# Performance work log

Hardware: AMD Instinct MI355X
Metric: run time of the kernel (lower is better)

## Reference

```python
import jax, jax.numpy as jnp
import numpy as np
import math

B, N, D = 2, 192, 256

def _linear_params(key, d_in, d_out):
    kw, kb = jax.random.split(key)
    scale = 1.0 / math.sqrt(d_in)
    W = jax.random.uniform(kw, (d_out, d_in), jnp.float32, -scale, scale)
    b = jax.random.uniform(kb, (d_out,), jnp.float32, -scale, scale)
    return W, b

def setup_inputs() -> dict:
    key = jax.random.key(0)
    ks = jax.random.split(key, 7)
    Edges = jax.random.normal(ks[0], (B, N * N, D), jnp.float32)
    Wq_w, Wq_b = _linear_params(ks[1], D, D)
    Wk_w, Wk_b = _linear_params(ks[2], D, D)
    Wv_w, Wv_b = _linear_params(ks[3], D, D)
    Wb_w, Wb_b = _linear_params(ks[4], D, 1)
    Wg_w, Wg_b = _linear_params(ks[5], D, D)
    Wo_w, Wo_b = _linear_params(ks[6], D, D)
    return {"Edges": Edges, "Wq_w": Wq_w, "Wq_b": Wq_b, "Wk_w": Wk_w, "Wk_b": Wk_b,
            "Wv_w": Wv_w, "Wv_b": Wv_b, "Wb_w": Wb_w, "Wb_b": Wb_b,
            "Wg_w": Wg_w, "Wg_b": Wg_b, "Wo_w": Wo_w, "Wo_b": Wo_b}

def reference(Edges, Wq_w, Wq_b, Wk_w, Wk_b, Wv_w, Wv_b, Wb_w, Wb_b, Wg_w, Wg_b, Wo_w, Wo_b):
    # Edges: [B, N*N, D]; dropout is identity in eval mode.
    Bb, NN, Dd = Edges.shape
    n = int(round(math.sqrt(NN)))
    q = (Edges @ Wq_w.T + Wq_b).reshape(Bb, n, n, Dd)
    k = (Edges @ Wk_w.T + Wk_b).reshape(Bb, n, n, Dd)
    v = (Edges @ Wv_w.T + Wv_b).reshape(Bb, n, n, Dd)
    bmat = (Edges @ Wb_w.T + Wb_b).reshape(Bb, n, n)          # b[b,i,l]
    g = jax.nn.sigmoid(Edges @ Wg_w.T + Wg_b)                  # [B, N*N, D]
    # row attention: q(i,j) . k(i,l) ; column attention: q(i,j) . k(l,j)
    scores = (jnp.einsum('bijd,bild->bijl', q, k)
              + jnp.einsum('bijd,bljd->bijl', q, k)) / math.sqrt(Dd)
    sym_bias = bmat + jnp.swapaxes(bmat, 1, 2)                 # b[i,l] + b[l,i]
    alpha = jax.nn.softmax(scores + sym_bias[:, :, None, :], axis=-1)  # [B,n,n,n]
    # first value contraction along rows; second term matches torch's
    # transpose-free add: out2[b,i,j,d] = sum_l alpha[b,j,i,l] v[b,l,i,d]
    o1 = jnp.einsum('bijl,bild->bijd', alpha, v)
    o2 = jnp.einsum('bjil,blid->bijd', alpha, v)
    out = g * (o1 + o2).reshape(Bb, NN, Dd)
    out = jax.nn.relu(out @ Wo_w.T + Wo_b)
    return out
```

## Files before the change

kernel.cpp:

```cpp
#include <hip/hip_runtime.h>
#include <hip/hip_bf16.h>

typedef __hip_bfloat16 bf16;
typedef unsigned short u16;
typedef __attribute__((ext_vector_type(8))) short bf16x8;
typedef __attribute__((ext_vector_type(4))) float f32x4;

#define NB   2
#define NG   192
#define DD   256
#define NN2  (NG*NG)
#define MT   (NB*NN2)

static __device__ __forceinline__ float bfu2f(u16 u){
    return __uint_as_float(((unsigned)u) << 16);
}
static __device__ __forceinline__ u16 f2bfu(float f){
    bf16 h = __float2bfloat16(f);
    return *(u16*)&h;
}

static __device__ __forceinline__ void gl_lds16(const void* g, void* l){
    __builtin_amdgcn_global_load_lds(
        (const __attribute__((address_space(1))) unsigned int*)g,
        (__attribute__((address_space(3))) unsigned int*)l, 16, 0, 0);
}
static __device__ __forceinline__ int swz3(int x){ return ((x ^ (x>>3)) & 7) << 3; }

__global__ __launch_bounds__(256) void k_cast_eb(
    const float* __restrict__ E, const float* __restrict__ Wb,
    const float* __restrict__ bb, u16* __restrict__ Eb, float* __restrict__ bm)
{
    const int t = threadIdx.x;
    size_t base = (size_t)blockIdx.x*2048 + t*8;
    float4 x = *(const float4*)(E+base);
    float4 y = *(const float4*)(E+base+4);
    ushort4 a; a.x=f2bfu(x.x); a.y=f2bfu(x.y); a.z=f2bfu(x.z); a.w=f2bfu(x.w);
    ushort4 b; b.x=f2bfu(y.x); b.y=f2bfu(y.y); b.z=f2bfu(y.z); b.w=f2bfu(y.w);
    *(ushort4*)(Eb+base)   = a;
    *(ushort4*)(Eb+base+4) = b;
    const int l32 = t & 31;
    float4 w0 = ((const float4*)Wb)[l32*2];
    float4 w1 = ((const float4*)Wb)[l32*2+1];
    float s = x.x*w0.x + x.y*w0.y + x.z*w0.z + x.w*w0.w
            + y.x*w1.x + y.y*w1.y + y.z*w1.z + y.w*w1.w;
    #pragma unroll
    for (int off=1; off<32; off<<=1) s += __shfl_xor(s, off);
    if (l32 == 0) bm[blockIdx.x*8 + (t>>5)] = s + bb[0];
}

__global__ __launch_bounds__(256) void k_cast_w(
    const float* __restrict__ Wq, const float* __restrict__ Wk,
    const float* __restrict__ Wv, const float* __restrict__ Wg,
    const float* __restrict__ Wo,
    const float* __restrict__ bq, const float* __restrict__ bk,
    const float* __restrict__ bv, const float* __restrict__ bg,
    u16* __restrict__ Wcat, u16* __restrict__ Wob, float* __restrict__ biascat)
{
    int e = blockIdx.x*256 + threadIdx.x;
    Wcat[e]          = f2bfu(Wq[e]);
    Wcat[65536 + e]  = f2bfu(Wk[e]);
    Wcat[131072 + e] = f2bfu(Wv[e]);
    Wcat[196608 + e] = f2bfu(Wg[e]);
    Wob[e]           = f2bfu(Wo[e]);
    if (e < 1024){
        int p = e>>8, r = e&255;
        const float* bp = p==0?bq : p==1?bk : p==2?bv : bg;
        biascat[e] = bp[r];
    }
}

static __device__ __forceinline__ void gemm128_dbuf(
    const u16* __restrict__ A, const u16* __restrict__ B,
    u16* As, u16* Bs, f32x4 acc[4][4], int t)
{
    const int lane = t & 63, w = t >> 6;
    const int wm = (w>>1)*64, wn = (w&1)*64;
    int offA[4], offB[4];
    #pragma unroll
    for (int f=0; f<4; f++){
        int ra = wm + f*16 + (lane&15);
        offA[f] = ra*32 + (((lane>>4) ^ ((ra>>1)&3)) << 3);
        int rb = wn + f*16 + (lane&15);
        offB[f] = rb*32 + (((lane>>4) ^ ((rb>>1)&3)) << 3);
    }
    auto stage = [&](int buf, int k0){
        #pragma unroll
        for (int it=0; it<2; it++){
            int c = it*256 + t;
            int row = c >> 2;
            int ks  = (c&3) ^ ((row>>1)&3);
            gl_lds16(A + (size_t)row*DD + k0 + ks*8, As + buf*4096 + c*8);
            gl_lds16(B + (size_t)row*DD + k0 + ks*8, Bs + buf*4096 + c*8);
        }
    };
    stage(0, 0);
    for (int ks=0; ks<8; ks++){
        if (ks<7){
            stage((ks+1)&1, (ks+1)*32);
            asm volatile("s_waitcnt vmcnt(4)" ::: "memory");
        } else {
            asm volatile("s_waitcnt vmcnt(0)" ::: "memory");
        }
        __builtin_amdgcn_s_barrier();
        const u16* Ab = As + (ks&1)*4096;
        const u16* Bb = Bs + (ks&1)*4096;
        bf16x8 a[4], b[4];
        #pragma unroll
        for (int f=0; f<4; f++) a[f] = *(const bf16x8*)(Ab + offA[f]);
        #pragma unroll
        for (int f=0; f<4; f++) b[f] = *(const bf16x8*)(Bb + offB[f]);
        #pragma unroll
        for (int mf=0; mf<4; mf++)
            #pragma unroll
            for (int nf=0; nf<4; nf++)
                acc[mf][nf] = __builtin_amdgcn_mfma_f32_16x16x32_bf16(a[mf], b[nf], acc[mf][nf], 0, 0, 0);
        __builtin_amdgcn_s_barrier();
    }
}

__global__ __launch_bounds__(256) void k_proj_mfma(
    const u16* __restrict__ Eb, const u16* __restrict__ Wcat,
    const float* __restrict__ biascat,
    u16* __restrict__ qb, u16* __restrict__ kb,
    u16* __restrict__ vb, u16* __restrict__ gb)
{
    __shared__ u16 As[2*4096];
    __shared__ u16 Bs[2*4096];
    const int blk = blockIdx.x;
    const int xj = blk & 7, xi = blk >> 3;
    const int m0 = (xj*72 + (xi>>3)) * 128;
    const int n0 = (xi & 7) * 128;
    const int t = threadIdx.x, lane = t&63, w = t>>6;
    f32x4 acc[4][4];
    #pragma unroll
    for (int i=0;i<4;i++)
        #pragma unroll
        for (int j=0;j<4;j++) acc[i][j] = f32x4{0.f,0.f,0.f,0.f};
    gemm128_dbuf(Eb + (size_t)m0*DD, Wcat + (size_t)n0*DD, As, Bs, acc, t);

    const int p = n0 >> 8;
    u16* outp = p==0?qb : p==1?kb : p==2?vb : gb;
    const int wm = (w>>1)*64, wn = (w&1)*64;
    #pragma unroll
    for (int mf=0; mf<4; mf++){
        int m = m0 + wm + mf*16 + (lane>>4)*4;
        #pragma unroll
        for (int nf=0; nf<4; nf++){
            int gn = n0 + wn + nf*16 + (lane&15);
            float bias = biascat[gn];
            int col = gn & 255;
            #pragma unroll
            for (int r=0; r<4; r++){
                float v = acc[mf][nf][r] + bias;
                if (p==3) v = 1.0f/(1.0f+__expf(-v));
                outp[(size_t)(m+r)*DD + col] = f2bfu(v);
            }
        }
    }
}

__global__ __launch_bounds__(256) void k_final_mfma(
    const u16* __restrict__ hb, const u16* __restrict__ Wob,
    const float* __restrict__ bo, float* __restrict__ out)
{
    __shared__ u16 As[2*4096];
    __shared__ u16 Bs[2*4096];
    const int blk = blockIdx.x;
    const int xj = blk & 7, xi = blk >> 3;
    const int m0 = (xj*72 + (xi>>1)) * 128;
    const int n0 = (xi & 1) * 128;
    const int t = threadIdx.x, lane = t&63, w = t>>6;
    f32x4 acc[4][4];
    #pragma unroll
    for (int i=0;i<4;i++)
        #pragma unroll
        for (int j=0;j<4;j++) acc[i][j] = f32x4{0.f,0.f,0.f,0.f};
    gemm128_dbuf(hb + (size_t)m0*DD, Wob + (size_t)n0*DD, As, Bs, acc, t);

    const int wm = (w>>1)*64, wn = (w&1)*64;
    #pragma unroll
    for (int mf=0; mf<4; mf++){
        int m = m0 + wm + mf*16 + (lane>>4)*4;
        #pragma unroll
        for (int nf=0; nf<4; nf++){
            int n = n0 + wn + nf*16 + (lane&15);
            float bias = bo[n];
            #pragma unroll
            for (int r=0; r<4; r++)
                out[(size_t)(m+r)*DD + n] = fmaxf(acc[mf][nf][r] + bias, 0.0f);
        }
    }
}

__global__ __launch_bounds__(512, 2) void k_scores(
    const u16* __restrict__ q, const u16* __restrict__ kmat,
    const float* __restrict__ bm,
    u16* __restrict__ S1, u16* __restrict__ S2T)
{
    __shared__ u16 As[2][NG*64];
    __shared__ u16 Bs[2][NG*64];
    const int MODE = blockIdx.y;
    const int z = blockIdx.x, b = z/NG, r = z%NG;
    const int t = threadIdx.x, lane = t&63, w = t>>6;
    const int wm = (w&3)*48, wn = (w>>2)*96;
    const size_t astr = MODE ? (size_t)NG*DD : (size_t)DD;
    const u16* Ab = MODE ? q    + ((size_t)b*NN2 + r)*DD : q    + ((size_t)b*NG + r)*NG*DD;
    const u16* Bb = MODE ? kmat + ((size_t)b*NN2 + r)*DD : kmat + ((size_t)b*NG + r)*NG*DD;

    f32x4 acc[3][6];
    #pragma unroll
    for (int i=0;i<3;i++)
        #pragma unroll
        for (int j=0;j<6;j++) acc[i][j] = f32x4{0.f,0.f,0.f,0.f};

    int offA[3], offB[6];
    #pragma unroll
    for (int mf=0; mf<3; mf++){
        int x = wm + mf*16 + (lane&15);
        offA[mf] = x*64 + (((lane>>4)<<3) ^ swz3(x));
    }
    #pragma unroll
    for (int nf=0; nf<6; nf++){
        int x = wn + nf*16 + (lane&15);
        offB[nf] = x*64 + (((lane>>4)<<3) ^ swz3(x));
    }

    auto stage = [&](int buf, int k0){
        #pragma unroll
        for (int rr=0; rr<3; rr++){
            int c = t + rr*512;
            int x = c>>3, l8e = (c&7)<<3;
            size_t ro = (size_t)x*astr + k0;
            gl_lds16(Ab + ro + (l8e ^ swz3(x)), &As[buf][c*8]);
            gl_lds16(Bb + ro + (l8e ^ swz3(x)), &Bs[buf][c*8]);
        }
    };

    stage(0, 0);
    for (int ks=0; ks<4; ks++){
        if (ks<3){
            stage((ks+1)&1, (ks+1)*64);
            asm volatile("s_waitcnt vmcnt(6)" ::: "memory");
        } else {
            asm volatile("s_waitcnt vmcnt(0)" ::: "memory");
        }
        __builtin_amdgcn_s_barrier();
        const u16* A = &As[ks&1][0];
        const u16* B = &Bs[ks&1][0];
        #pragma unroll
        for (int kk=0; kk<2; kk++){
            bf16x8 a[3];
            #pragma unroll
            for (int mf=0; mf<3; mf++) a[mf] = *(const bf16x8*)(A + (offA[mf]^(kk<<5)));
            #pragma unroll
            for (int nf=0; nf<6; nf++){
                bf16x8 bf = *(const bf16x8*)(B + (offB[nf]^(kk<<5)));
                #pragma unroll
                for (int mf=0; mf<3; mf++)
                    acc[mf][nf] = __builtin_amdgcn_mfma_f32_16x16x32_bf16(a[mf], bf, acc[mf][nf], 0, 0, 0);
            }
        }
        __builtin_amdgcn_s_barrier();
    }

    u16* outb = (MODE ? S2T : S1) + ((size_t)b*NG + r)*NN2;
    const float* bmb = bm + (size_t)b*NN2;
    #pragma unroll
    for (int mf=0; mf<3; mf++){
        #pragma unroll
        for (int nf=0; nf<6; nf++){
            int lcol = wn + nf*16 + (lane&15);
            float bias = MODE ? 0.f : (bmb[(size_t)r*NG + lcol] + bmb[(size_t)lcol*NG + r]);
            #pragma unroll
            for (int r4=0; r4<4; r4++){
                int x = wm + mf*16 + (lane>>4)*4 + r4;
                outb[(size_t)x*NG + lcol] = f2bfu(acc[mf][nf][r4]*0.0625f + bias);
            }
        }
    }
}

__global__ __launch_bounds__(256) void k_softmax(
    const u16* __restrict__ S1, const u16* __restrict__ S2T,
    u16* __restrict__ alpha)
{
    int rr   = blockIdx.x*4 + (threadIdx.x >> 6);
    int lane = threadIdx.x & 63;
    int b = blockIdx.y;
    int i = rr / NG, j = rr % NG;
    const u16* r1 = S1  + ((size_t)b*NN2 + rr)*NG;
    const u16* r2 = S2T + ((size_t)b*NN2 + (size_t)j*NG + i)*NG;
    float vals[3];
    float mx = -1e30f;
    #pragma unroll
    for (int tt=0; tt<3; tt++){
        int l = lane + tt*64;
        float s = bfu2f(r1[l]) + bfu2f(r2[l]);
        vals[tt] = s;
        mx = fmaxf(mx, s);
    }
    #pragma unroll
    for (int off=32; off; off>>=1) mx = fmaxf(mx, __shfl_xor(mx, off));
    float sum = 0.f;
    #pragma unroll
    for (int tt=0; tt<3; tt++){ vals[tt] = __expf(vals[tt]-mx); sum += vals[tt]; }
    #pragma unroll
    for (int off=32; off; off>>=1) sum += __shfl_xor(sum, off);
    float inv = 1.0f/sum;
    u16* arow1 = alpha + ((size_t)b*NN2 + rr)*NG;
    #pragma unroll
    for (int tt=0; tt<3; tt++)
        arow1[lane + tt*64] = f2bfu(vals[tt]*inv);
}

__global__ __launch_bounds__(512, 4) void k_attnout(
    const u16* __restrict__ alpha,
    const u16* __restrict__ vb, const u16* __restrict__ gb, u16* __restrict__ hb)
{
    __shared__ u16 AsL[2][NG*64];
    __shared__ u16 Vs[128*64];
    const int z = blockIdx.x;
    const int xcd = z & 7, s = z >> 3;
    const int bi = xcd*48 + (s>>1), dh = s & 1;
    const int b = bi/NG, i = bi%NG;
    const int dbase = dh*128;
    const int t = threadIdx.x, lane = t&63, w = t>>6;
    const int wm = (w&1)*96, wn = (w>>1)*32;

    const u16* Abase0 = alpha + (size_t)bi*NN2;
    const u16* Abase1 = alpha + ((size_t)b*NN2 + i)*NG;
    const u16* V0 = vb + (size_t)bi*NG*DD + dbase;
    const u16* V1 = vb + ((size_t)b*NG*NG + i)*DD + dbase;

    f32x4 acc[6][2];
    #pragma unroll
    for (int m=0;m<6;m++)
        #pragma unroll
        for (int n=0;n<2;n++) acc[m][n] = f32x4{0.f,0.f,0.f,0.f};

    int offA[6], offB[2];
    #pragma unroll
    for (int mf=0; mf<6; mf++){
        int j = wm + mf*16 + (lane&15);
        offA[mf] = j*64 + (((lane>>4)<<3) ^ swz3(j));
    }
    #pragma unroll
    for (int nf=0; nf<2; nf++){
        int d = wn + nf*16 + (lane&15);
        offB[nf] = d*64 + (((lane>>4)<<3) ^ swz3(d));
    }

    int4 vr[2];
    auto stageA = [&](int u, int buf){
        const u16* Ab = (u>=3) ? Abase1 : Abase0;
        const size_t astrd = (u>=3) ? (size_t)NN2 : (size_t)NG;
        int ls = (u>=3 ? u-3 : u)*64;
        #pragma unroll
        for (int rr=0; rr<3; rr++){
            int c = t + rr*512;
            int j = c>>3, l8e = (c&7)<<3;
            gl_lds16(Ab + (size_t)j*astrd + ls + (l8e ^ swz3(j)), &AsL[buf][c*8]);
        }
    };
    auto loadV = [&](int u){
        int p = (u>=3), ls = (u>=3 ? u-3 : u)*64;
        #pragma unroll
        for (int rr=0; rr<2; rr++){
            int c = t + rr*512;
            int l = ls + (c>>4), d0 = (c&15)*8;
            const u16* src = p ? (V1 + (size_t)l*NG*DD + d0) : (V0 + (size_t)l*DD + d0);
            vr[rr] = *(const int4*)src;
        }
    };

    stageA(0, 0);
    loadV(0);
    for (int u=0; u<6; u++){
        #pragma unroll
        for (int rr=0; rr<2; rr++){
            int c = t + rr*512;
            int l = c>>4;
            l &= 63;
            int d0 = (c&15)*8, c3 = c&7;
            ushort* vp = (ushort*)&vr[rr];
            #pragma unroll
            for (int qd=0; qd<8; qd++)
                Vs[(d0+qd)*64 + (l ^ ((qd^c3)<<3))] = vp[qd];
        }
        if (u<5){ stageA(u+1, (u+1)&1); loadV(u+1); }
        asm volatile("s_waitcnt lgkmcnt(0)" ::: "memory");
        __builtin_amdgcn_s_barrier();
        const u16* A = &AsL[u&1][0];
        #pragma unroll
        for (int kk=0; kk<2; kk++){
            bf16x8 bfr[2];
            #pragma unroll
            for (int nf=0; nf<2; nf++) bfr[nf] = *(const bf16x8*)(Vs + (offB[nf]^(kk<<5)));
            #pragma unroll
            for (int mf=0; mf<6; mf++){
                bf16x8 afr = *(const bf16x8*)(A + (offA[mf]^(kk<<5)));
                acc[mf][0] = __builtin_amdgcn_mfma_f32_16x16x32_bf16(afr, bfr[0], acc[mf][0], 0, 0, 0);
                acc[mf][1] = __builtin_amdgcn_mfma_f32_16x16x32_bf16(afr, bfr[1], acc[mf][1], 0, 0, 0);
            }
        }
        __builtin_amdgcn_s_barrier();
    }

    #pragma unroll
    for (int mf=0; mf<6; mf++){
        #pragma unroll
        for (int nf=0; nf<2; nf++){
            #pragma unroll
            for (int r4=0; r4<4; r4++){
                int j = wm + mf*16 + (lane>>4)*4 + r4;
                int d = dbase + wn + nf*16 + (lane&15);
                size_t idx = ((size_t)bi*NG + j)*DD + d;
                hb[idx] = f2bfu(bfu2f(gb[idx]) * acc[mf][nf][r4]);
            }
        }
    }
}

extern "C" void kernel_launch(void* const* d_in, const int* in_sizes, int n_in,
                              void* d_out, int out_size, void* d_ws, size_t ws_size,
                              hipStream_t stream)
{
    const float* E  = (const float*)d_in[0];
    const float* Wq = (const float*)d_in[1];  const float* bq = (const float*)d_in[2];
    const float* Wk = (const float*)d_in[3];  const float* bk = (const float*)d_in[4];
    const float* Wv = (const float*)d_in[5];  const float* bv = (const float*)d_in[6];
    const float* Wb = (const float*)d_in[7];  const float* bb = (const float*)d_in[8];
    const float* Wg = (const float*)d_in[9];  const float* bg = (const float*)d_in[10];
    const float* Wo = (const float*)d_in[11]; const float* bo = (const float*)d_in[12];
    float* out = (float*)d_out;

    const size_t BF = (size_t)MT*DD*2;
    const size_t SC = (size_t)NB*NG*NG*NG*4;
    char* ws = (char*)d_ws;
    u16* Eb  = (u16*)ws;
    u16* S1  = (u16*)ws;
    u16* S2T = (u16*)(ws + SC/2);
    u16* hb  = (u16*)ws;
    u16* qb = (u16*)(ws + SC);           u16* alpha = qb;
    u16* kb = (u16*)(ws + SC + BF);
    u16* vb = (u16*)(ws + SC + 2*BF);
    u16* gb = (u16*)(ws + SC + 3*BF);
    size_t tail = SC + 4*BF;
    float* bm      = (float*)(ws + tail); tail += (size_t)MT*4;
    u16* Wcat      = (u16*)(ws + tail);   tail += (size_t)1024*DD*2;
    u16* Wob       = (u16*)(ws + tail);   tail += (size_t)DD*DD*2;
    float* biascat = (float*)(ws + tail); tail += 1024*4;
    (void)ws_size;

    k_cast_w   <<<dim3(256), 256, 0, stream>>>(Wq,Wk,Wv,Wg,Wo, bq,bk,bv,bg, Wcat, Wob, biascat);
    k_cast_eb  <<<dim3(9216), 256, 0, stream>>>(E, Wb, bb, Eb, bm);
    k_proj_mfma<<<dim3(4608), 256, 0, stream>>>(Eb, Wcat, biascat, qb, kb, vb, gb);
    k_scores   <<<dim3(NB*NG, 2), 512, 0, stream>>>(qb, kb, bm, S1, S2T);
    k_softmax  <<<dim3(NN2/4, NB), 256, 0, stream>>>(S1, S2T, alpha);
    k_attnout  <<<dim3(NB*NG*2), 512, 0, stream>>>(alpha, vb, gb, hb);
    k_final_mfma<<<dim3(1152), 256, 0, stream>>>(hb, Wob, bo, out);
}
```

Measured before the change: 223.0 us.

## Widen projection GEMM tile to 128x256 with inlined double-buffered pipeline

The QKVG projection kernel now computes a 128x256 output tile per block instead of 128x128, so each block covers one full projection. This halves the block count and the number of times the A (edge) tile is reloaded from global memory. The k-loop is inlined with its own staging lambda and vmcnt waits, and launch_bounds requests two blocks per CU. In exchange each thread holds twice as many accumulators and the block uses more LDS, which raises register pressure and may lower occupancy.

```diff
diff --git a/kernel.cpp b/kernel.cpp
--- a/kernel.cpp
+++ b/kernel.cpp
@@ -119,37 +119,90 @@
     }
 }
 
-__global__ __launch_bounds__(256) void k_proj_mfma(
+__global__ __launch_bounds__(256, 2) void k_proj_mfma(
     const u16* __restrict__ Eb, const u16* __restrict__ Wcat,
     const float* __restrict__ biascat,
     u16* __restrict__ qb, u16* __restrict__ kb,
     u16* __restrict__ vb, u16* __restrict__ gb)
 {
     __shared__ u16 As[2*4096];
-    __shared__ u16 Bs[2*4096];
+    __shared__ u16 Bs[2*8192];
     const int blk = blockIdx.x;
     const int xj = blk & 7, xi = blk >> 3;
-    const int m0 = (xj*72 + (xi>>3)) * 128;
-    const int n0 = (xi & 7) * 128;
+    const int m0 = (xj*72 + (xi>>2)) * 128;
+    const int n0 = (xi & 3) * 256;
     const int t = threadIdx.x, lane = t&63, w = t>>6;
-    f32x4 acc[4][4];
+    const int wm = (w>>1)*64, wn = (w&1)*128;
+
+    int offA[4], offB[8];
+    #pragma unroll
+    for (int f=0; f<4; f++){
+        int ra = wm + f*16 + (lane&15);
+        offA[f] = ra*32 + (((lane>>4) ^ ((ra>>1)&3)) << 3);
+    }
+    #pragma unroll
+    for (int f=0; f<8; f++){
+        int rb = wn + f*16 + (lane&15);
+        offB[f] = rb*32 + (((lane>>4) ^ ((rb>>1)&3)) << 3);
+    }
+    const u16* A = Eb   + (size_t)m0*DD;
+    const u16* B = Wcat + (size_t)n0*DD;
+    auto stage = [&](int buf, int k0){
+        #pragma unroll
+        for (int it=0; it<2; it++){
+            int c = it*256 + t;
+            int row = c >> 2;
+            int ks  = (c&3) ^ ((row>>1)&3);
+            gl_lds16(A + (size_t)row*DD + k0 + ks*8, As + buf*4096 + c*8);
+        }
+        #pragma unroll
+        for (int it=0; it<4; it++){
+            int c = it*256 + t;
+            int row = c >> 2;
+            int ks  = (c&3) ^ ((row>>1)&3);
+            gl_lds16(B + (size_t)row*DD + k0 + ks*8, Bs + buf*8192 + c*8);
+        }
+    };
+
+    f32x4 acc[4][8];
     #pragma unroll
     for (int i=0;i<4;i++)
         #pragma unroll
-        for (int j=0;j<4;j++) acc[i][j] = f32x4{0.f,0.f,0.f,0.f};
-    gemm128_dbuf(Eb + (size_t)m0*DD, Wcat + (size_t)n0*DD, As, Bs, acc, t);
+        for (int j=0;j<8;j++) acc[i][j] = f32x4{0.f,0.f,0.f,0.f};
+
+    stage(0, 0);
+    for (int ks=0; ks<8; ks++){
+        if (ks<7){
+            stage((ks+1)&1, (ks+1)*32);
+            asm volatile("s_waitcnt vmcnt(6)" ::: "memory");
+        } else {
+            asm volatile("s_waitcnt vmcnt(0)" ::: "memory");
+        }
+        __builtin_amdgcn_s_barrier();
+        const u16* Ab = As + (ks&1)*4096;
+        const u16* Bb = Bs + (ks&1)*8192;
+        bf16x8 a[4], b[8];
+        #pragma unroll
+        for (int f=0; f<4; f++) a[f] = *(const bf16x8*)(Ab + offA[f]);
+        #pragma unroll
+        for (int f=0; f<8; f++) b[f] = *(const bf16x8*)(Bb + offB[f]);
+        #pragma unroll
+        for (int mf=0; mf<4; mf++)
+            #pragma unroll
+            for (int nf=0; nf<8; nf++)
+                acc[mf][nf] = __builtin_amdgcn_mfma_f32_16x16x32_bf16(a[mf], b[nf], acc[mf][nf], 0, 0, 0);
+        __builtin_amdgcn_s_barrier();
+    }
 
     const int p = n0 >> 8;
     u16* outp = p==0?qb : p==1?kb : p==2?vb : gb;
-    const int wm = (w>>1)*64, wn = (w&1)*64;
     #pragma unroll
     for (int mf=0; mf<4; mf++){
         int m = m0 + wm + mf*16 + (lane>>4)*4;
         #pragma unroll
-        for (int nf=0; nf<4; nf++){
-            int gn = n0 + wn + nf*16 + (lane&15);
-            float bias = biascat[gn];
-            int col = gn & 255;
+        for (int nf=0; nf<8; nf++){
+            int col = wn + nf*16 + (lane&15);
+            float bias = biascat[n0 + col];
             #pragma unroll
             for (int r=0; r<4; r++){
                 float v = acc[mf][nf][r] + bias;
@@ -455,7 +508,7 @@
 
     k_cast_w   <<<dim3(256), 256, 0, stream>>>(Wq,Wk,Wv,Wg,Wo, bq,bk,bv,bg, Wcat, Wob, biascat);
     k_cast_eb  <<<dim3(9216), 256, 0, stream>>>(E, Wb, bb, Eb, bm);
-    k_proj_mfma<<<dim3(4608), 256, 0, stream>>>(Eb, Wcat, biascat, qb, kb, vb, gb);
+    k_proj_mfma<<<dim3(2304), 256, 0, stream>>>(Eb, Wcat, biascat, qb, kb, vb, gb);
     k_scores   <<<dim3(NB*NG, 2), 512, 0, stream>>>(qb, kb, bm, S1, S2T);
     k_softmax  <<<dim3(NN2/4, NB), 256, 0, stream>>>(S1, S2T, alpha);
     k_attnout  <<<dim3(NB*NG*2), 512, 0, stream>>>(alpha, vb, gb, hb);
```

After: 234.5 us. 5.1% more time.
